# Kernel tuning notes

Measured on AMD Instinct MI355X. Metric: run time of the kernel, lower is better.

## Reference

```python
import jax, jax.numpy as jnp
import numpy as np

B, S, D_EMBED, D_HIDDEN = 4, 256, 300, 300
C = 5.0  # frozen tanh-scaling constant


def setup_inputs() -> dict:
    key = jax.random.key(0)
    ks = jax.random.split(key, 8)
    w = 0.05  # ~xavier scale for 300x300
    return {
        "inputs": jax.random.normal(ks[0], (B, S, D_EMBED), jnp.float32),
        "rep_mask": jax.random.randint(ks[1], (B, S), 0, 2, jnp.int32),
        "W_fc": jax.random.normal(ks[2], (D_HIDDEN, D_EMBED), jnp.float32) * w,
        "b_fc": jnp.zeros((D_HIDDEN,), jnp.float32),
        "W1": jax.random.normal(ks[3], (D_HIDDEN, D_HIDDEN), jnp.float32) * w,
        "W2": jax.random.normal(ks[4], (D_HIDDEN, D_HIDDEN), jnp.float32) * w,
        "b1": jnp.zeros((D_HIDDEN,), jnp.float32),
        "W_f1": jax.random.normal(ks[5], (D_HIDDEN, D_HIDDEN), jnp.float32) * w,
        "W_f2": jax.random.normal(ks[6], (D_HIDDEN, D_HIDDEN), jnp.float32) * w,
        "b_f": jnp.zeros((D_HIDDEN,), jnp.float32),
    }


def _disa_fwd(inputs, rep_mask_f, W_fc, b_fc, W1, W2, b1, W_f1, W_f2, b_f):
    n_seq = inputs.shape[1]
    # forward direction mask: attend to strictly later positions (triu, diag=1)
    direct = jnp.triu(jnp.ones((n_seq, n_seq), inputs.dtype), k=1)
    # mask[b,i,j] = rep_mask[b,j] * direct[i,j], shape [B,S,S,1]
    mask = (rep_mask_f[:, None, :] * direct[None]) [..., None]

    rep_map = jax.nn.elu(jnp.einsum('bse,he->bsh', inputs, W_fc) + b_fc)  # [B,S,D]
    dep = jnp.einsum('bsh,gh->bsg', rep_map, W1)   # dependent (token j)
    head = jnp.einsum('bsh,gh->bsg', rep_map, W2)  # head (token i)

    # logits[b,i,j,d]
    logits = C * jnp.tanh((dep[:, None, :, :] + head[:, :, None, :] + b1) / C)

    # hand-rolled masked softmax over dim=2 (j), faithful to original
    masked = logits * mask
    mx = jnp.max(masked, axis=2, keepdims=True)
    exps = jnp.exp(masked - mx) * mask
    sums = jnp.sum(exps, axis=2, keepdims=True)
    sums = sums + (sums == 0).astype(logits.dtype)
    attn = (exps / (sums + 1e-20)) * mask

    attn_result = jnp.sum(attn * rep_map[:, None, :, :], axis=2)  # [B,S,D]

    gate = jax.nn.sigmoid(
        jnp.einsum('bsh,gh->bsg', rep_map, W_f1)
        + jnp.einsum('bsh,gh->bsg', attn_result, W_f2)
        + b_f
    )
    out = gate * rep_map + (1.0 - gate) * attn_result
    return out * rep_mask_f[..., None]


def reference(inputs, rep_mask, W_fc, b_fc, W1, W2, b1, W_f1, W_f2, b_f):
    rep_mask_f = rep_mask.astype(inputs.dtype)
    return _disa_fwd(inputs, rep_mask_f, W_fc, b_fc, W1, W2, b1, W_f1, W_f2, b_f)
```

## Files before the change

### kernel.cpp

```cpp
#include <hip/hip_runtime.h>
#include <hip/hip_bf16.h>

#define Dx 300

#define OFF_REP    0
#define OFF_DEP    307200
#define OFF_HEAD   614400
#define OFF_ATTN   921600
#define U_BASE     1228800
#define REPB       0
#define ATB        327680
#define WPACK      655360
#define WP1        655360
#define WP2        757760
#define WPF1       860160
#define WPF2       962560
#define SYNC_FOFF  2000000

#define NBLK 320

typedef __attribute__((ext_vector_type(8))) short short8;
typedef __attribute__((ext_vector_type(4))) float f32x4;

union S8 { unsigned int u[4]; unsigned short s[8]; short8 v; };

__device__ __forceinline__ float bf2f(unsigned short u) {
    union { unsigned int i; float f; } v; v.i = ((unsigned int)u) << 16; return v.f;
}
__device__ __forceinline__ unsigned short f2bf(float x) {
    union { float f; unsigned int i; } u; u.f = x;
    return (unsigned short)((u.i + 0x8000u) >> 16);
}
__device__ __forceinline__ int detect_bf16(const void* w) {
    const unsigned short* u = (const unsigned short*)w;
    int ok = 1;
    #pragma unroll
    for (int t = 0; t < 64; ++t) { float v = bf2f(u[t]); ok &= (fabsf(v) < 1.0f) ? 1 : 0; }
    return ok;
}
__device__ __forceinline__ float ldf(const void* p, int idx, int isbf) {
    return isbf ? bf2f(((const unsigned short*)p)[idx]) : ((const float*)p)[idx];
}

__device__ __forceinline__ void st_wt_f32(float* p, float v) {
    asm volatile("global_store_dword %0, %1, off sc0 sc1"
                 :: "v"(p), "v"(v) : "memory");
}
__device__ __forceinline__ void st_wt_u16(unsigned short* p, unsigned short v) {
    unsigned int vv = v;
    asm volatile("global_store_short %0, %1, off sc0 sc1"
                 :: "v"(p), "v"(vv) : "memory");
}
__device__ __forceinline__ void st_wt_b64(void* p, unsigned long long v) {
    asm volatile("global_store_dwordx2 %0, %1, off sc0 sc1"
                 :: "v"(p), "v"(v) : "memory");
}

__device__ __forceinline__ void load8f(const float* rowp, int kb, int kmax,
                                       int valid, float* x) {
    if (valid && kb + 8 <= kmax) {
        float4 a = *(const float4*)(rowp + kb);
        float4 b = *(const float4*)(rowp + kb + 4);
        x[0]=a.x; x[1]=a.y; x[2]=a.z; x[3]=a.w;
        x[4]=b.x; x[5]=b.y; x[6]=b.z; x[7]=b.w;
    } else {
        #pragma unroll
        for (int j = 0; j < 8; ++j) {
            int k = kb + j;
            x[j] = (valid && k < kmax) ? rowp[k] : 0.f;
        }
    }
}
__device__ __forceinline__ short8 pack8(const float* x) {
    S8 H;
    #pragma unroll
    for (int p = 0; p < 4; ++p) {
        union { float f; unsigned int i; } a, b;
        a.f = x[2*p]; b.f = x[2*p+1];
        H.u[p] = ((a.i + 0x8000u) >> 16) | ((b.i + 0x8000u) & 0xFFFF0000u);
    }
    return H.v;
}
__device__ __forceinline__ short8 load8bf(const unsigned short* rowp, int kb,
                                          int kmax, int valid) {
    S8 R;
    if (valid && kb + 8 <= kmax) {
        ushort4 a = *(const ushort4*)(rowp + kb);
        ushort4 b = *(const ushort4*)(rowp + kb + 4);
        R.s[0]=a.x; R.s[1]=a.y; R.s[2]=a.z; R.s[3]=a.w;
        R.s[4]=b.x; R.s[5]=b.y; R.s[6]=b.z; R.s[7]=b.w;
    } else {
        #pragma unroll
        for (int j = 0; j < 8; ++j) {
            int k = kb + j;
            R.s[j] = (valid && k < kmax) ? rowp[k] : (unsigned short)0;
        }
    }
    return R.v;
}
__device__ __forceinline__ short8 loadB(const void* W, int row, int kb, int isbf,
                                        int valid) {
    if (isbf) return load8bf((const unsigned short*)W + row * 300, kb, 300, valid);
    float t[8];
    load8f((const float*)W + row * 300, kb, 300, valid, t);
    return pack8(t);
}

#define AG __HIP_MEMORY_SCOPE_AGENT
__device__ __forceinline__ int xcd_id() {
    int x;
    asm volatile("s_getreg_b32 %0, hwreg(HW_REG_XCC_ID)" : "=s"(x));
    return x & 7;
}

__device__ __forceinline__ void gbar(float* ws, int idx) {
    __syncthreads();
    if (threadIdx.x == 0) {
        int* base  = (int*)(ws + SYNC_FOFF) + idx * 2048;
        int* xcnt  = base;
        int* xflag = base + 8 * 64;
        const int xid = xcd_id();
        int t2 = __hip_atomic_fetch_add(xcnt + xid * 64, 1, __ATOMIC_RELAXED, AG);
        if (t2 == 0) {
            int t = 0;
            for (;;) {
                int s = 0;
                #pragma unroll
                for (int k = 0; k < 8; ++k)
                    s += __hip_atomic_load(xcnt + k * 64, __ATOMIC_RELAXED, AG);
                if (s >= NBLK) break;
                __builtin_amdgcn_s_sleep(1);
                if (++t > 400000) break;
            }
            __hip_atomic_store(xflag + xid * 64, 1, __ATOMIC_RELAXED, AG);
        } else {
            int t = 0;
            while (__hip_atomic_load(xflag + xid * 64, __ATOMIC_RELAXED, AG) == 0) {
                __builtin_amdgcn_s_sleep(2);
                if (++t > 400000) break;
            }
        }
        asm volatile("" ::: "memory");
    }
    __syncthreads();
}

__global__ __launch_bounds__(320, 4) void k_fused(
        const void* __restrict__ Xv, const int* __restrict__ mask,
        const void* __restrict__ Wfc, const void* __restrict__ bfc,
        const void* __restrict__ W1,  const void* __restrict__ W2,
        const void* __restrict__ b1v, const void* __restrict__ Wf1,
        const void* __restrict__ Wf2, const void* __restrict__ bfv,
        float* __restrict__ ws, void* __restrict__ outv) {
    __shared__ int s_isbf;
    __shared__ unsigned short vlist[256];
    __shared__ int s_cnt, s_st0, s_st1;

    const int tid = threadIdx.x;
    const int blk = blockIdx.x;
    if (tid == 0) s_isbf = detect_bf16(Wfc);
    __syncthreads();
    const int isbf = s_isbf;
    unsigned short* U = (unsigned short*)(ws + U_BASE);

    {
        const int g0 = blk * 1280 + tid * 4;
        const int mi = g0 / 102400;
        const int rem = g0 - mi * 102400;
        const int row = rem / 320, k0 = rem - row * 320;
        const void* src = (mi == 0) ? W1 : (mi == 1) ? W2 : (mi == 2) ? Wf1 : Wf2;
        union { ushort4 s4; unsigned long long u64; } o;
        unsigned short* op = (unsigned short*)&o.s4;
        #pragma unroll
        for (int j = 0; j < 4; ++j) {
            float v = (row < 300 && k0 + j < 300) ? ldf(src, row * 300 + k0 + j, isbf) : 0.f;
            op[j] = f2bf(v);
        }
        st_wt_b64(U + WPACK + g0, o.u64);
    }
    if (tid < 256) {
        const int w = tid >> 6, l = tid & 63;
        const int mt = blk / 5, nt = blk % 5;
        const int m0 = mt * 16, lm = l & 15, koff = (l >> 4) * 8;
        const int nrow = nt * 64 + w * 16 + lm;
        const int bval = nrow < 300;
        const int ncl = bval ? nrow : 0;
        f32x4 acc = {0.f, 0.f, 0.f, 0.f};
        if (isbf) {
            const unsigned short* Xp = (const unsigned short*)Xv + (m0 + lm) * 300;
            #pragma unroll
            for (int ks = 0; ks < 10; ++ks) {
                short8 a = load8bf(Xp, ks*32 + koff, 300, 1);
                short8 b = loadB(Wfc, ncl, ks*32 + koff, 1, bval);
                acc = __builtin_amdgcn_mfma_f32_16x16x32_bf16(a, b, acc, 0, 0, 0);
            }
        } else {
            const float* Xp = (const float*)Xv + (m0 + lm) * 300;
            #pragma unroll
            for (int ks = 0; ks < 10; ++ks) {
                float t[8]; load8f(Xp, ks*32 + koff, 300, 1, t);
                short8 a = pack8(t);
                short8 b = loadB(Wfc, ncl, ks*32 + koff, 0, bval);
                acc = __builtin_amdgcn_mfma_f32_16x16x32_bf16(a, b, acc, 0, 0, 0);
            }
        }
        if (bval) {
            float bb = ldf(bfc, nrow, isbf);
            #pragma unroll
            for (int r = 0; r < 4; ++r) {
                int mg = m0 + (l >> 4) * 4 + r;
                float v = acc[r] + bb;
                v = v > 0.f ? v : (__expf(v) - 1.f);
                st_wt_f32(ws + OFF_REP + mg * 300 + nrow, v);
                st_wt_u16(U + REPB + mg * 320 + nrow, f2bf(v));
            }
        } else {
            #pragma unroll
            for (int r = 0; r < 4; ++r) {
                int mg = m0 + (l >> 4) * 4 + r;
                st_wt_u16(U + REPB + mg * 320 + nrow, 0);
            }
        }
    }
    gbar(ws, 0);

    if (tid < 256) {
        const int w = tid >> 6, l = tid & 63;
        const int lm = l & 15, koff = (l >> 4) * 8;
        #pragma unroll
        for (int u = blk; u < 640; u += 320) {
            const int mt = u / 10, nt = u % 10;
            const int m0 = mt * 16;
            const int ng = nt * 64 + w * 16 + lm;
            const int wsel = ng < 320;
            const int wrow = wsel ? ng : ng - 320;
            const unsigned short* ap = U + REPB + (m0 + lm) * 320 + koff;
            const unsigned short* bp = U + (wsel ? WP1 : WP2) + wrow * 320 + koff;
            f32x4 acc = {0.f, 0.f, 0.f, 0.f};
            #pragma unroll
            for (int ks = 0; ks < 10; ++ks) {
                short8 a = *(const short8*)(ap + ks * 32);
                short8 b = *(const short8*)(bp + ks * 32);
                acc = __builtin_amdgcn_mfma_f32_16x16x32_bf16(a, b, acc, 0, 0, 0);
            }
            if (ng < 300) {
                float bb = ldf(b1v, ng, isbf);
                #pragma unroll
                for (int r = 0; r < 4; ++r) {
                    int mg = m0 + (l >> 4) * 4 + r;
                    st_wt_f32(ws + OFF_DEP + mg * 300 + ng,
                              __expf(0.4f * (acc[r] + bb)));
                }
            } else if (ng >= 320 && ng < 620) {
                #pragma unroll
                for (int r = 0; r < 4; ++r) {
                    int mg = m0 + (l >> 4) * 4 + r;
                    st_wt_f32(ws + OFF_HEAD + mg * 300 + (ng - 320), acc[r]);
                }
            }
        }
    }
    gbar(ws, 1);

    for (int u = blk; u < 512; u += 320) {
        const int b = u >> 7;
        const int tile = u & 127;
        const int uu = tile >> 1;
        const int i0 = (tile & 1) ? (254 - 2 * uu) : (2 * uu);
        const int base = b * 256;
        const int mv0 = mask[base + i0] != 0;
        const int mv1 = mask[base + i0 + 1] != 0;
        __syncthreads();
        if ((mv0 | mv1) && tid < 64) {
            int basec = 0, st0 = 0, st1 = 0;
            #pragma unroll
            for (int c = 0; c < 4; ++c) {
                const int j = c * 64 + tid;
                const int mv = mask[base + j] != 0;
                unsigned long long bal = __ballot(mv);
                int pos = basec + __popcll(bal & ((1ull << tid) - 1ull));
                if (mv) vlist[pos] = (unsigned short)j;
                if (tid == 0) {
                    int lim0 = i0 - c * 64;
                    if (lim0 >= 0)
                        st0 += __popcll(bal & (lim0 >= 63 ? ~0ull : ((2ull << lim0) - 1ull)));
                    int lim1 = i0 + 1 - c * 64;
                    if (lim1 >= 0)
                        st1 += __popcll(bal & (lim1 >= 63 ? ~0ull : ((2ull << lim1) - 1ull)));
                }
                basec += __popcll(bal);
            }
            if (tid == 0) { s_cnt = basec; s_st0 = st0; s_st1 = st1; }
        }
        __syncthreads();
        const int d = tid;
        if (d >= 300) {
            st_wt_u16(U + ATB + (base + i0) * 320 + d, 0);
            st_wt_u16(U + ATB + (base + i0 + 1) * 320 + d, 0);
        } else if (mv0 & mv1) {
            const int cnt = s_cnt, st0 = s_st0, st1 = s_st1;
            const float* headp = ws + OFF_HEAD;
            const float hv0 = headp[(base + i0) * Dx + d];
            const float hv1 = headp[(base + i0 + 1) * Dx + d];
            const float pw0 = __expf(0.4f * hv0);
            const float pw1 = __expf(0.4f * hv1);
            const float* ep = ws + OFF_DEP + base * Dx + d;
            const float* rp = ws + OFF_REP + base * Dx + d;
            float s0 = 0.f, r0 = 0.f, s1 = 0.f, r1 = 0.f;
            if (st1 > st0) {
                const int j = vlist[st0];
                float ex = ep[j * Dx];
                float rv = rp[j * Dx];
                float u0 = fmaf(ex, pw0, 1.0f);
                float e0 = __expf(-10.0f * __builtin_amdgcn_rcpf(u0));
                s0 += e0; r0 = fmaf(e0, rv, r0);
            }
            #pragma unroll 4
            for (int t = st1; t < cnt; ++t) {
                const int j = vlist[t];
                float ex = ep[j * Dx];
                float rv = rp[j * Dx];
                float u0 = fmaf(ex, pw0, 1.0f);
                float u1 = fmaf(ex, pw1, 1.0f);
                float e0 = __expf(-10.0f * __builtin_amdgcn_rcpf(u0));
                float e1 = __expf(-10.0f * __builtin_amdgcn_rcpf(u1));
                s0 += e0; r0 = fmaf(e0, rv, r0);
                s1 += e1; r1 = fmaf(e1, rv, r1);
            }
            const float den0 = s0 + (s0 == 0.f ? 1.f : 0.f) + 1e-20f;
            const float den1 = s1 + (s1 == 0.f ? 1.f : 0.f) + 1e-20f;
            const float a0 = r0 / den0, a1 = r1 / den1;
            st_wt_f32(ws + OFF_ATTN + (base + i0) * Dx + d,     a0);
            st_wt_f32(ws + OFF_ATTN + (base + i0 + 1) * Dx + d, a1);
            st_wt_u16(U + ATB + (base + i0) * 320 + d,     f2bf(a0));
            st_wt_u16(U + ATB + (base + i0 + 1) * 320 + d, f2bf(a1));
        } else if (mv0 | mv1) {
            const int cnt = s_cnt;
            const int ia  = mv0 ? i0 : (i0 + 1);
            const int sta = mv0 ? s_st0 : s_st1;
            const float hv = (ws + OFF_HEAD)[(base + ia) * Dx + d];
            const float pw = __expf(0.4f * hv);
            const float* ep = ws + OFF_DEP + base * Dx + d;
            const float* rp = ws + OFF_REP + base * Dx + d;
            float s = 0.f, r = 0.f;
            #pragma unroll 4
            for (int t = sta; t < cnt; ++t) {
                const int j = vlist[t];
                float ex = ep[j * Dx];
                float rv = rp[j * Dx];
                float u0 = fmaf(ex, pw, 1.0f);
                float e  = __expf(-10.0f * __builtin_amdgcn_rcpf(u0));
                s += e; r = fmaf(e, rv, r);
            }
            const float den = s + (s == 0.f ? 1.f : 0.f) + 1e-20f;
            const float a = r / den;
            st_wt_f32(ws + OFF_ATTN + (base + ia) * Dx + d, a);
            st_wt_u16(U + ATB + (base + ia) * 320 + d, f2bf(a));
        }
    }
    gbar(ws, 2);

    if (tid < 256) {
        const int w = tid >> 6, l = tid & 63;
        const int mt = blk / 5, nt = blk % 5;
        const int m0 = mt * 16, lm = l & 15, koff = (l >> 4) * 8;
        const int nrow = nt * 64 + w * 16 + lm;
        const unsigned short* a1p = U + REPB + (m0 + lm) * 320 + koff;
        const unsigned short* a2p = U + ATB  + (m0 + lm) * 320 + koff;
        const unsigned short* b1p = U + WPF1 + nrow * 320 + koff;
        const unsigned short* b2p = U + WPF2 + nrow * 320 + koff;
        f32x4 acc = {0.f, 0.f, 0.f, 0.f};
        #pragma unroll
        for (int ks = 0; ks < 10; ++ks) {
            short8 a = *(const short8*)(a1p + ks * 32);
            short8 b = *(const short8*)(b1p + ks * 32);
            acc = __builtin_amdgcn_mfma_f32_16x16x32_bf16(a, b, acc, 0, 0, 0);
        }
        #pragma unroll
        for (int ks = 0; ks < 10; ++ks) {
            short8 a = *(const short8*)(a2p + ks * 32);
            short8 b = *(const short8*)(b2p + ks * 32);
            acc = __builtin_amdgcn_mfma_f32_16x16x32_bf16(a, b, acc, 0, 0, 0);
        }
        if (nrow < 300) {
            float bb = ldf(bfv, nrow, isbf);
            #pragma unroll
            for (int r = 0; r < 4; ++r) {
                int mg = m0 + (l >> 4) * 4 + r;
                float res = 0.f;
                if (mask[mg]) {
                    float gp = acc[r] + bb;
                    float gate = 1.0f / (1.0f + __expf(-gp));
                    float rv = ws[OFF_REP  + mg * 300 + nrow];
                    float av = ws[OFF_ATTN + mg * 300 + nrow];
                    res = gate * rv + (1.0f - gate) * av;
                }
                if (isbf) ((__hip_bfloat16*)outv)[mg * 300 + nrow] = __float2bfloat16(res);
                else      ((float*)outv)[mg * 300 + nrow] = res;
            }
        }
    }
}

extern "C" void kernel_launch(void* const* d_in, const int* in_sizes, int n_in,
                              void* d_out, int out_size, void* d_ws, size_t ws_size,
                              hipStream_t stream) {
    const void* X   = d_in[0];
    const int*  msk = (const int*)d_in[1];
    const void* Wfc = d_in[2];
    const void* bfc = d_in[3];
    const void* W1  = d_in[4];
    const void* W2  = d_in[5];
    const void* b1  = d_in[6];
    const void* Wf1 = d_in[7];
    const void* Wf2 = d_in[8];
    const void* bfv = d_in[9];
    float* ws = (float*)d_ws;

    hipMemsetAsync((char*)d_ws + (size_t)SYNC_FOFF * sizeof(float), 0, 24576, stream);

    hipLaunchKernelGGL(k_fused, dim3(NBLK), dim3(320), 0, stream,
                       X, msk, Wfc, bfc, W1, W2, b1, Wf1, Wf2, bfv, ws, d_out);
}
```

Before: 133.9 us.

## Split fused persistent kernel into two launches with wider grids and interleaved dep/rep

Replaces the single 320-block persistent kernel with three grid barriers by two kernels: k_a (640 blocks) does the weight packing, the fc projection and the dep/head projections, and k_b (512 blocks) does the attention scan and the gate GEMM. The kernel boundary replaces one software grid barrier, and each work unit now gets its own block instead of looping. The exp(dep) and rep values are interleaved into float2 pairs so the inner attention loop issues one 8-byte load per element instead of two scattered loads, and the unroll is raised to 8. The remaining in-kernel barrier in k_b now spins over 512 co-resident blocks, which relies on all of them being resident at once, and the extra launch adds its own overhead.

```diff
diff --git a/kernel.cpp b/kernel.cpp
--- a/kernel.cpp
+++ b/kernel.cpp
@@ -3,21 +3,19 @@
 
 #define Dx 300
 
-#define OFF_REP    0
-#define OFF_DEP    307200
-#define OFF_HEAD   614400
-#define OFF_ATTN   921600
-#define U_BASE     1228800
-#define REPB       0
-#define ATB        327680
-#define WPACK      655360
-#define WP1        655360
-#define WP2        757760
-#define WPF1       860160
-#define WPF2       962560
-#define SYNC_FOFF  2000000
-
-#define NBLK 320
+#define REPF   0
+#define ED     307200
+#define HEADF  921600
+#define U_BASE 1228800
+#define REPB   0
+#define ATB    327680
+#define WPACK  655360
+#define WP1    655360
+#define WP2    757760
+#define WPF1   860160
+#define WPF2   962560
+#define ATTNF  1761280
+#define SYNC_FOFF 2100000
 
 typedef __attribute__((ext_vector_type(8))) short short8;
 typedef __attribute__((ext_vector_type(4))) float f32x4;
@@ -51,8 +49,8 @@
     asm volatile("global_store_short %0, %1, off sc0 sc1"
                  :: "v"(p), "v"(vv) : "memory");
 }
-__device__ __forceinline__ void st_wt_b64(void* p, unsigned long long v) {
-    asm volatile("global_store_dwordx2 %0, %1, off sc0 sc1"
+__device__ __forceinline__ void st_wt_u32(void* p, unsigned int v) {
+    asm volatile("global_store_dword %0, %1, off sc0 sc1"
                  :: "v"(p), "v"(v) : "memory");
 }
 
@@ -112,8 +110,7 @@
     asm volatile("s_getreg_b32 %0, hwreg(HW_REG_XCC_ID)" : "=s"(x));
     return x & 7;
 }
-
-__device__ __forceinline__ void gbar(float* ws, int idx) {
+__device__ __forceinline__ void gbar(float* ws, int idx, int nblk) {
     __syncthreads();
     if (threadIdx.x == 0) {
         int* base  = (int*)(ws + SYNC_FOFF) + idx * 2048;
@@ -128,7 +125,7 @@
                 #pragma unroll
                 for (int k = 0; k < 8; ++k)
                     s += __hip_atomic_load(xcnt + k * 64, __ATOMIC_RELAXED, AG);
-                if (s >= NBLK) break;
+                if (s >= nblk) break;
                 __builtin_amdgcn_s_sleep(1);
                 if (++t > 400000) break;
             }
@@ -145,17 +142,13 @@
     __syncthreads();
 }
 
-__global__ __launch_bounds__(320, 4) void k_fused(
-        const void* __restrict__ Xv, const int* __restrict__ mask,
-        const void* __restrict__ Wfc, const void* __restrict__ bfc,
-        const void* __restrict__ W1,  const void* __restrict__ W2,
-        const void* __restrict__ b1v, const void* __restrict__ Wf1,
-        const void* __restrict__ Wf2, const void* __restrict__ bfv,
-        float* __restrict__ ws, void* __restrict__ outv) {
+__global__ __launch_bounds__(320, 4) void k_a(
+        const void* __restrict__ Xv, const void* __restrict__ Wfc,
+        const void* __restrict__ bfc, const void* __restrict__ W1,
+        const void* __restrict__ W2,  const void* __restrict__ b1v,
+        const void* __restrict__ Wf1, const void* __restrict__ Wf2,
+        float* __restrict__ ws) {
     __shared__ int s_isbf;
-    __shared__ unsigned short vlist[256];
-    __shared__ int s_cnt, s_st0, s_st1;
-
     const int tid = threadIdx.x;
     const int blk = blockIdx.x;
     if (tid == 0) s_isbf = detect_bf16(Wfc);
@@ -164,21 +157,17 @@
     unsigned short* U = (unsigned short*)(ws + U_BASE);
 
     {
-        const int g0 = blk * 1280 + tid * 4;
+        const int g0 = blk * 640 + tid * 2;
         const int mi = g0 / 102400;
         const int rem = g0 - mi * 102400;
         const int row = rem / 320, k0 = rem - row * 320;
         const void* src = (mi == 0) ? W1 : (mi == 1) ? W2 : (mi == 2) ? Wf1 : Wf2;
-        union { ushort4 s4; unsigned long long u64; } o;
-        unsigned short* op = (unsigned short*)&o.s4;
-        #pragma unroll
-        for (int j = 0; j < 4; ++j) {
-            float v = (row < 300 && k0 + j < 300) ? ldf(src, row * 300 + k0 + j, isbf) : 0.f;
-            op[j] = f2bf(v);
-        }
-        st_wt_b64(U + WPACK + g0, o.u64);
-    }
-    if (tid < 256) {
+        float v0 = (row < 300 && k0     < 300) ? ldf(src, row * 300 + k0,     isbf) : 0.f;
+        float v1 = (row < 300 && k0 + 1 < 300) ? ldf(src, row * 300 + k0 + 1, isbf) : 0.f;
+        unsigned int pk = (unsigned int)f2bf(v0) | ((unsigned int)f2bf(v1) << 16);
+        st_wt_u32(U + WPACK + g0, pk);
+    }
+    if (blk < 320 && tid < 256) {
         const int w = tid >> 6, l = tid & 63;
         const int mt = blk / 5, nt = blk % 5;
         const int m0 = mt * 16, lm = l & 15, koff = (l >> 4) * 8;
@@ -211,7 +200,8 @@
                 int mg = m0 + (l >> 4) * 4 + r;
                 float v = acc[r] + bb;
                 v = v > 0.f ? v : (__expf(v) - 1.f);
-                st_wt_f32(ws + OFF_REP + mg * 300 + nrow, v);
+                ws[REPF + mg * 300 + nrow] = v;
+                ws[ED + (mg * 300 + nrow) * 2 + 1] = v;
                 st_wt_u16(U + REPB + mg * 320 + nrow, f2bf(v));
             }
         } else {
@@ -222,55 +212,65 @@
             }
         }
     }
-    gbar(ws, 0);
+    gbar(ws, 0, 640);
 
     if (tid < 256) {
         const int w = tid >> 6, l = tid & 63;
         const int lm = l & 15, koff = (l >> 4) * 8;
+        const int u = blk;
+        const int mt = u / 10, nt = u % 10;
+        const int m0 = mt * 16;
+        const int ng = nt * 64 + w * 16 + lm;
+        const int wsel = ng < 320;
+        const int wrow = wsel ? ng : ng - 320;
+        const unsigned short* ap = U + REPB + (m0 + lm) * 320 + koff;
+        const unsigned short* bp = U + (wsel ? WP1 : WP2) + wrow * 320 + koff;
+        f32x4 acc = {0.f, 0.f, 0.f, 0.f};
         #pragma unroll
-        for (int u = blk; u < 640; u += 320) {
-            const int mt = u / 10, nt = u % 10;
-            const int m0 = mt * 16;
-            const int ng = nt * 64 + w * 16 + lm;
-            const int wsel = ng < 320;
-            const int wrow = wsel ? ng : ng - 320;
-            const unsigned short* ap = U + REPB + (m0 + lm) * 320 + koff;
-            const unsigned short* bp = U + (wsel ? WP1 : WP2) + wrow * 320 + koff;
-            f32x4 acc = {0.f, 0.f, 0.f, 0.f};
-            #pragma unroll
-            for (int ks = 0; ks < 10; ++ks) {
-                short8 a = *(const short8*)(ap + ks * 32);
-                short8 b = *(const short8*)(bp + ks * 32);
-                acc = __builtin_amdgcn_mfma_f32_16x16x32_bf16(a, b, acc, 0, 0, 0);
-            }
-            if (ng < 300) {
-                float bb = ldf(b1v, ng, isbf);
-                #pragma unroll
-                for (int r = 0; r < 4; ++r) {
-                    int mg = m0 + (l >> 4) * 4 + r;
-                    st_wt_f32(ws + OFF_DEP + mg * 300 + ng,
-                              __expf(0.4f * (acc[r] + bb)));
-                }
-            } else if (ng >= 320 && ng < 620) {
-                #pragma unroll
-                for (int r = 0; r < 4; ++r) {
-                    int mg = m0 + (l >> 4) * 4 + r;
-                    st_wt_f32(ws + OFF_HEAD + mg * 300 + (ng - 320), acc[r]);
-                }
-            }
-        }
-    }
-    gbar(ws, 1);
-
-    for (int u = blk; u < 512; u += 320) {
-        const int b = u >> 7;
-        const int tile = u & 127;
+        for (int ks = 0; ks < 10; ++ks) {
+            short8 a = *(const short8*)(ap + ks * 32);
+            short8 b = *(const short8*)(bp + ks * 32);
+            acc = __builtin_amdgcn_mfma_f32_16x16x32_bf16(a, b, acc, 0, 0, 0);
+        }
+        if (ng < 300) {
+            float bb = ldf(b1v, ng, isbf);
+            #pragma unroll
+            for (int r = 0; r < 4; ++r) {
+                int mg = m0 + (l >> 4) * 4 + r;
+                ws[ED + (mg * 300 + ng) * 2] = __expf(0.4f * (acc[r] + bb));
+            }
+        } else if (ng >= 320 && ng < 620) {
+            #pragma unroll
+            for (int r = 0; r < 4; ++r) {
+                int mg = m0 + (l >> 4) * 4 + r;
+                ws[HEADF + mg * 300 + (ng - 320)] = acc[r];
+            }
+        }
+    }
+}
+
+__global__ __launch_bounds__(320, 4) void k_b(
+        const int* __restrict__ mask, const void* __restrict__ Wfc,
+        const void* __restrict__ bfv, float* __restrict__ ws,
+        void* __restrict__ outv) {
+    __shared__ int s_isbf;
+    __shared__ unsigned short vlist[256];
+    __shared__ int s_cnt, s_st0, s_st1;
+    const int tid = threadIdx.x;
+    const int blk = blockIdx.x;
+    if (tid == 0) s_isbf = detect_bf16(Wfc);
+    __syncthreads();
+    const int isbf = s_isbf;
+    unsigned short* U = (unsigned short*)(ws + U_BASE);
+
+    {
+        const int b = blk >> 7;
+        const int tile = blk & 127;
         const int uu = tile >> 1;
         const int i0 = (tile & 1) ? (254 - 2 * uu) : (2 * uu);
         const int base = b * 256;
         const int mv0 = mask[base + i0] != 0;
         const int mv1 = mask[base + i0 + 1] != 0;
-        __syncthreads();
         if ((mv0 | mv1) && tid < 64) {
             int basec = 0, st0 = 0, st1 = 0;
             #pragma unroll
@@ -299,68 +299,62 @@
             st_wt_u16(U + ATB + (base + i0 + 1) * 320 + d, 0);
         } else if (mv0 & mv1) {
             const int cnt = s_cnt, st0 = s_st0, st1 = s_st1;
-            const float* headp = ws + OFF_HEAD;
-            const float hv0 = headp[(base + i0) * Dx + d];
-            const float hv1 = headp[(base + i0 + 1) * Dx + d];
+            const float hv0 = ws[HEADF + (base + i0) * Dx + d];
+            const float hv1 = ws[HEADF + (base + i0 + 1) * Dx + d];
             const float pw0 = __expf(0.4f * hv0);
             const float pw1 = __expf(0.4f * hv1);
-            const float* ep = ws + OFF_DEP + base * Dx + d;
-            const float* rp = ws + OFF_REP + base * Dx + d;
+            const float2* ep2 = ((const float2*)(ws + ED)) + base * Dx + d;
             float s0 = 0.f, r0 = 0.f, s1 = 0.f, r1 = 0.f;
             if (st1 > st0) {
                 const int j = vlist[st0];
-                float ex = ep[j * Dx];
-                float rv = rp[j * Dx];
-                float u0 = fmaf(ex, pw0, 1.0f);
+                float2 v = ep2[j * Dx];
+                float u0 = fmaf(v.x, pw0, 1.0f);
                 float e0 = __expf(-10.0f * __builtin_amdgcn_rcpf(u0));
-                s0 += e0; r0 = fmaf(e0, rv, r0);
-            }
-            #pragma unroll 4
+                s0 += e0; r0 = fmaf(e0, v.y, r0);
+            }
+            #pragma unroll 8
             for (int t = st1; t < cnt; ++t) {
                 const int j = vlist[t];
-                float ex = ep[j * Dx];
-                float rv = rp[j * Dx];
-                float u0 = fmaf(ex, pw0, 1.0f);
-                float u1 = fmaf(ex, pw1, 1.0f);
+                float2 v = ep2[j * Dx];
+                float u0 = fmaf(v.x, pw0, 1.0f);
+                float u1 = fmaf(v.x, pw1, 1.0f);
                 float e0 = __expf(-10.0f * __builtin_amdgcn_rcpf(u0));
                 float e1 = __expf(-10.0f * __builtin_amdgcn_rcpf(u1));
-                s0 += e0; r0 = fmaf(e0, rv, r0);
-                s1 += e1; r1 = fmaf(e1, rv, r1);
+                s0 += e0; r0 = fmaf(e0, v.y, r0);
+                s1 += e1; r1 = fmaf(e1, v.y, r1);
             }
             const float den0 = s0 + (s0 == 0.f ? 1.f : 0.f) + 1e-20f;
             const float den1 = s1 + (s1 == 0.f ? 1.f : 0.f) + 1e-20f;
             const float a0 = r0 / den0, a1 = r1 / den1;
-            st_wt_f32(ws + OFF_ATTN + (base + i0) * Dx + d,     a0);
-            st_wt_f32(ws + OFF_ATTN + (base + i0 + 1) * Dx + d, a1);
+            st_wt_f32(ws + ATTNF + (base + i0) * Dx + d,     a0);
+            st_wt_f32(ws + ATTNF + (base + i0 + 1) * Dx + d, a1);
             st_wt_u16(U + ATB + (base + i0) * 320 + d,     f2bf(a0));
             st_wt_u16(U + ATB + (base + i0 + 1) * 320 + d, f2bf(a1));
         } else if (mv0 | mv1) {
             const int cnt = s_cnt;
             const int ia  = mv0 ? i0 : (i0 + 1);
             const int sta = mv0 ? s_st0 : s_st1;
-            const float hv = (ws + OFF_HEAD)[(base + ia) * Dx + d];
+            const float hv = ws[HEADF + (base + ia) * Dx + d];
             const float pw = __expf(0.4f * hv);
-            const float* ep = ws + OFF_DEP + base * Dx + d;
-            const float* rp = ws + OFF_REP + base * Dx + d;
+            const float2* ep2 = ((const float2*)(ws + ED)) + base * Dx + d;
             float s = 0.f, r = 0.f;
-            #pragma unroll 4
+            #pragma unroll 8
             for (int t = sta; t < cnt; ++t) {
                 const int j = vlist[t];
-                float ex = ep[j * Dx];
-                float rv = rp[j * Dx];
-                float u0 = fmaf(ex, pw, 1.0f);
+                float2 v = ep2[j * Dx];
+                float u0 = fmaf(v.x, pw, 1.0f);
                 float e  = __expf(-10.0f * __builtin_amdgcn_rcpf(u0));
-                s += e; r = fmaf(e, rv, r);
+                s += e; r = fmaf(e, v.y, r);
             }
             const float den = s + (s == 0.f ? 1.f : 0.f) + 1e-20f;
             const float a = r / den;
-            st_wt_f32(ws + OFF_ATTN + (base + ia) * Dx + d, a);
+            st_wt_f32(ws + ATTNF + (base + ia) * Dx + d, a);
             st_wt_u16(U + ATB + (base + ia) * 320 + d, f2bf(a));
         }
     }
-    gbar(ws, 2);
-
-    if (tid < 256) {
+    gbar(ws, 1, 512);
+
+    if (blk < 320 && tid < 256) {
         const int w = tid >> 6, l = tid & 63;
         const int mt = blk / 5, nt = blk % 5;
         const int m0 = mt * 16, lm = l & 15, koff = (l >> 4) * 8;
@@ -391,8 +385,8 @@
                 if (mask[mg]) {
                     float gp = acc[r] + bb;
                     float gate = 1.0f / (1.0f + __expf(-gp));
-                    float rv = ws[OFF_REP  + mg * 300 + nrow];
-                    float av = ws[OFF_ATTN + mg * 300 + nrow];
+                    float rv = ws[REPF  + mg * 300 + nrow];
+                    float av = ws[ATTNF + mg * 300 + nrow];
                     res = gate * rv + (1.0f - gate) * av;
                 }
                 if (isbf) ((__hip_bfloat16*)outv)[mg * 300 + nrow] = __float2bfloat16(res);
@@ -417,8 +411,10 @@
     const void* bfv = d_in[9];
     float* ws = (float*)d_ws;
 
-    hipMemsetAsync((char*)d_ws + (size_t)SYNC_FOFF * sizeof(float), 0, 24576, stream);
-
-    hipLaunchKernelGGL(k_fused, dim3(NBLK), dim3(320), 0, stream,
-                       X, msk, Wfc, bfc, W1, W2, b1, Wf1, Wf2, bfv, ws, d_out);
-}
+    hipMemsetAsync((char*)d_ws + (size_t)SYNC_FOFF * sizeof(float), 0, 16384, stream);
+
+    hipLaunchKernelGGL(k_a, dim3(640), dim3(320), 0, stream,
+                       X, Wfc, bfc, W1, W2, b1, Wf1, Wf2, ws);
+    hipLaunchKernelGGL(k_b, dim3(512), dim3(320), 0, stream,
+                       msk, Wfc, bfv, ws, d_out);
+}
```

After: 127.2 us. 5.0% less time.
